# Performance work log

Hardware: AMD Instinct MI355X
Metric: run time of the kernel (lower is better)

## Reference

```python
import jax, jax.numpy as jnp
import numpy as np

N = 50000
P = 200000
L = 6
IN_DIM = 128
OUT_DIM = 128
HEADS = 4


def setup_inputs() -> dict:
    key = jax.random.key(0)
    ks = jax.random.split(key, 7)
    x = jax.random.normal(ks[0], (N, IN_DIM), dtype=jnp.float32)
    path_list = jax.random.randint(ks[1], (P, L), 0, N, dtype=jnp.int64)
    s = 0.1
    w_ih = jax.random.normal(ks[2], (3 * OUT_DIM, IN_DIM), dtype=jnp.float32) * s
    w_hh = jax.random.normal(ks[3], (3 * OUT_DIM, OUT_DIM), dtype=jnp.float32) * s
    b_ih = jax.random.normal(ks[4], (3 * OUT_DIM,), dtype=jnp.float32) * s
    b_hh = jax.random.normal(ks[5], (3 * OUT_DIM,), dtype=jnp.float32) * s
    a = jax.random.uniform(ks[6], (OUT_DIM, HEADS), dtype=jnp.float32) * 2.0 - 1.0
    return {"x": x, "path_list": path_list, "w_ih": w_ih, "w_hh": w_hh,
            "b_ih": b_ih, "b_hh": b_hh, "a": a}


def _gru_final_hidden(feats, w_ih, w_hh, b_ih, b_hh):
    # feats: [P, L, in_dim]; PyTorch GRU cell semantics, h0 = 0.
    out_dim = w_hh.shape[1]
    p = feats.shape[0]

    def step(h, xt):
        gi = xt @ w_ih.T + b_ih          # [P, 3*out]
        gh = h @ w_hh.T + b_hh           # [P, 3*out]
        ir, iz, i_n = jnp.split(gi, 3, axis=-1)
        hr, hz, h_n = jnp.split(gh, 3, axis=-1)
        r = jax.nn.sigmoid(ir + hr)
        z = jax.nn.sigmoid(iz + hz)
        n_cand = jnp.tanh(i_n + r * h_n)
        h_new = (1.0 - z) * n_cand + z * h
        return h_new, None

    h0 = jnp.zeros((p, out_dim), feats.dtype)
    xs = jnp.swapaxes(feats, 0, 1)       # [L, P, in_dim]
    h, _ = jax.lax.scan(step, h0, xs)
    return h                              # [P, out_dim]


def reference(x, path_list, w_ih, w_hh, b_ih, b_hh, a):
    n, out_dim = x.shape[0], w_hh.shape[1]
    heads = a.shape[1]
    # F.embedding(path_list, x): gather path features [P, L, in_dim]
    feats = x[path_list]
    path_emb = _gru_final_hidden(feats, w_ih, w_hh, b_ih, b_hh)       # [P, out]
    # unnormalized attention per head
    att_un = jnp.exp(jax.nn.leaky_relu(path_emb @ a, negative_slope=0.2))  # [P, H]
    row = path_list[:, -1]                                             # owner node of each path
    # M @ att_un : segment-sum over owner nodes
    att_sum = jax.ops.segment_sum(att_un, row, num_segments=n)         # [N, H]
    # M.t() @ (1/att_sum) : gather back to paths
    att_low = (1.0 / att_sum)[row]                                     # [P, H]
    att_n = att_un * att_low                                           # [P, H]
    # reshape(-1,1).repeat(1,out).reshape(P,-1): each head's scalar repeated out_dim times
    att_rep = jnp.repeat(att_n, out_dim, axis=1)                       # [P, H*out]
    emb_rep = jnp.tile(path_emb, (1, heads))                           # [P, H*out]
    path_att_emb = att_rep * emb_rep
    node_att_emb = jax.ops.segment_sum(path_att_emb, row, num_segments=n)  # [N, H*out]
    return node_att_emb
```

## Files before the change

### kernel.cpp

```cpp
#include <hip/hip_runtime.h>
#include <hip/hip_bf16.h>
#include <math.h>

#define NN 50000
#define PP 200000
#define LL 6
#define DD 128
#define HH 4

#define TM 32
#define NT 512
#define HPAD 132

typedef __attribute__((ext_vector_type(8))) short short8;
typedef __attribute__((ext_vector_type(4))) float f32x4;

struct f3 { float x, y, z; };

__device__ __forceinline__ unsigned short f2bf(float v) {
    __hip_bfloat16 h = __float2bfloat16(v);
    return *(unsigned short*)&h;
}
__device__ __forceinline__ float bf2f(unsigned short u) {
    union { unsigned int i; float f; } c; c.i = ((unsigned int)u) << 16; return c.f;
}
__device__ __forceinline__ float fast_rcp(float x) { return __builtin_amdgcn_rcpf(x); }
__device__ __forceinline__ float fast_sigmoid(float x) {
    return fast_rcp(1.f + __expf(-x));
}
__device__ __forceinline__ float fast_tanh(float x) {
    float e = __expf(-2.f * fabsf(x));
    float t = (1.f - e) * fast_rcp(1.f + e);
    return copysignf(t, x);
}

__global__ void prep_w_kernel(const float* __restrict__ w_hh,
                              unsigned short* __restrict__ whb) {
    int i = blockIdx.x * 256 + threadIdx.x;
    if (i < 3 * DD * DD) whb[i] = f2bf(w_hh[i]);
}

__global__ void histo_kernel(const int* __restrict__ path_list,
                             int* __restrict__ cnt) {
    int p = blockIdx.x * 256 + threadIdx.x;
    if (p < PP) atomicAdd(&cnt[path_list[p * LL + (LL - 1)]], 1);
}

__global__ void scan_kernel(const int* __restrict__ cnt,
                            int* __restrict__ offs,
                            int* __restrict__ cursor) {
    __shared__ int ls[256];
    const int t = threadIdx.x;
    const int chunk = (NN + 255) / 256;
    int s = 0;
    for (int j = 0; j < chunk; ++j) {
        int i = t + j * 256;
        if (i < NN) s += cnt[i];
    }
    ls[t] = s; __syncthreads();
    for (int off = 1; off < 256; off <<= 1) {
        int v = (t >= off) ? ls[t - off] : 0;
        __syncthreads();
        ls[t] += v;
        __syncthreads();
    }
    int run = (t == 0) ? 0 : ls[t - 1];
    for (int j = 0; j < chunk; ++j) {
        int i = t + j * 256;
        if (i < NN) { offs[i] = run; cursor[i] = run; run += cnt[i]; }
    }
}

__global__ void scatter_kernel(const int* __restrict__ path_list,
                               int* __restrict__ cursor,
                               int* __restrict__ sorted) {
    int p = blockIdx.x * 256 + threadIdx.x;
    if (p < PP) {
        int row = path_list[p * LL + (LL - 1)];
        int k = atomicAdd(&cursor[row], 1);
        sorted[k] = p;
    }
}

__global__ __launch_bounds__(512, 2)
void gi_gemm_kernel(const float* __restrict__ x,
                    const float* __restrict__ w_ih,
                    const float* __restrict__ b_ih,
                    const float* __restrict__ b_hh,
                    float* __restrict__ gi)
{
    const int tid  = threadIdx.x;
    const int lane = tid & 63;
    const int wave = tid >> 6;
    const int lcol = lane & 15;
    const int quad = lane >> 4;
    const int ko   = quad * 8;
    const int d    = wave * 16 + lcol;
    const int r0   = blockIdx.x * 64;

    short8 B[3][4];
    float bias[3];
    #pragma unroll
    for (int c = 0; c < 3; ++c) {
        int col = c * 128 + d;
        #pragma unroll
        for (int ks = 0; ks < 4; ++ks) {
            const float4* src = (const float4*)(w_ih + (size_t)col * 128 + ks * 32 + ko);
            float4 f0 = src[0], f1 = src[1];
            short8 b;
            b[0] = (short)f2bf(f0.x); b[1] = (short)f2bf(f0.y);
            b[2] = (short)f2bf(f0.z); b[3] = (short)f2bf(f0.w);
            b[4] = (short)f2bf(f1.x); b[5] = (short)f2bf(f1.y);
            b[6] = (short)f2bf(f1.z); b[7] = (short)f2bf(f1.w);
            B[c][ks] = b;
        }
        bias[c] = b_ih[col] + ((c < 2) ? b_hh[col] : 0.f);
    }

    f32x4 acc[3][4];
    #pragma unroll
    for (int c = 0; c < 3; ++c)
        #pragma unroll
        for (int rt = 0; rt < 4; ++rt)
            acc[c][rt] = (f32x4){bias[c], bias[c], bias[c], bias[c]};

    #pragma unroll
    for (int ks = 0; ks < 4; ++ks) {
        #pragma unroll
        for (int rt = 0; rt < 4; ++rt) {
            int row = r0 + rt * 16 + lcol;
            if (row >= NN) row = NN - 1;
            const float4* src = (const float4*)(x + (size_t)row * 128 + ks * 32 + ko);
            float4 f0 = src[0], f1 = src[1];
            short8 av;
            av[0] = (short)f2bf(f0.x); av[1] = (short)f2bf(f0.y);
            av[2] = (short)f2bf(f0.z); av[3] = (short)f2bf(f0.w);
            av[4] = (short)f2bf(f1.x); av[5] = (short)f2bf(f1.y);
            av[6] = (short)f2bf(f1.z); av[7] = (short)f2bf(f1.w);
            acc[0][rt] = __builtin_amdgcn_mfma_f32_16x16x32_bf16(av, B[0][ks], acc[0][rt], 0, 0, 0);
            acc[1][rt] = __builtin_amdgcn_mfma_f32_16x16x32_bf16(av, B[1][ks], acc[1][rt], 0, 0, 0);
            acc[2][rt] = __builtin_amdgcn_mfma_f32_16x16x32_bf16(av, B[2][ks], acc[2][rt], 0, 0, 0);
        }
    }

    #pragma unroll
    for (int rt = 0; rt < 4; ++rt)
        #pragma unroll
        for (int rr = 0; rr < 4; ++rr) {
            int row = r0 + rt * 16 + quad * 4 + rr;
            if (row < NN) {
                float* o = gi + (size_t)row * 384 + d * 3;
                o[0] = acc[0][rt][rr];
                o[1] = acc[1][rt][rr];
                o[2] = acc[2][rt][rr];
            }
        }
}

__global__ __launch_bounds__(NT, 4)
void gru_att_kernel(const float* __restrict__ gi,
                    const int*   __restrict__ path_list,
                    const unsigned short* __restrict__ whb,
                    const float* __restrict__ b_hh,
                    const float* __restrict__ a,
                    float* __restrict__ att_sum,
                    unsigned short* __restrict__ emb,
                    float* __restrict__ att_un_g)
{
    __shared__ __align__(16) unsigned char smem[25856];
    unsigned short* hs0    = (unsigned short*)smem;
    unsigned short* hs1    = (unsigned short*)(smem + 8192);
    float*          hs_f   = (float*)smem;
    float*          red_s  = (float*)(smem + 16896);
    int*            nodes_s= (int*)(smem + 25088);

    const int tid  = threadIdx.x;
    const int lane = tid & 63;
    const int wave = tid >> 6;
    const int lcol = lane & 15;
    const int quad = lane >> 4;
    const int d    = wave * 16 + lcol;
    const int p0   = blockIdx.x * TM;
    const int ko   = quad * 8;

    short8 Bh[3][4];
    #pragma unroll
    for (int c = 0; c < 3; ++c)
        #pragma unroll
        for (int ks = 0; ks < 4; ++ks)
            Bh[c][ks] = *(const short8*)(whb + (size_t)(c * DD + d) * DD + ks * 32 + ko);
    const float bhn = b_hh[d + 256];

    for (int i = tid; i < TM * LL; i += NT) nodes_s[i] = path_list[(size_t)p0 * LL + i];
    if (tid < TM * DD / 8)
        ((uint4*)hs0)[tid] = make_uint4(0u, 0u, 0u, 0u);

    float hreg[8];
    #pragma unroll
    for (int i = 0; i < 8; ++i) hreg[i] = 0.f;

    __syncthreads();

    #pragma unroll 1
    for (int t = 0; t < LL; ++t) {
        unsigned short* hr = (t & 1) ? hs1 : hs0;
        unsigned short* hw = (t & 1) ? hs0 : hs1;

        f3 g[8];
        #pragma unroll
        for (int rt = 0; rt < 2; ++rt)
            #pragma unroll
            for (int r = 0; r < 4; ++r) {
                const int p = rt * 16 + quad * 4 + r;
                const int node = nodes_s[p * LL + t];
                g[rt * 4 + r] = *(const f3*)(gi + (size_t)node * 384 + d * 3);
            }

        f32x4 accR[2], accZ[2], accH[2];
        #pragma unroll
        for (int rt = 0; rt < 2; ++rt) {
            accR[rt] = (f32x4){0.f, 0.f, 0.f, 0.f};
            accZ[rt] = (f32x4){0.f, 0.f, 0.f, 0.f};
            accH[rt] = (f32x4){bhn, bhn, bhn, bhn};
        }

        #pragma unroll
        for (int ks = 0; ks < 4; ++ks) {
            const int kb = ks * 4 + quad;
            #pragma unroll
            for (int rt = 0; rt < 2; ++rt) {
                const int p = rt * 16 + lcol;
                short8 ah = *(const short8*)(hr + p * DD + ((kb ^ lcol) * 8));
                accR[rt] = __builtin_amdgcn_mfma_f32_16x16x32_bf16(ah, Bh[0][ks], accR[rt], 0, 0, 0);
                accZ[rt] = __builtin_amdgcn_mfma_f32_16x16x32_bf16(ah, Bh[1][ks], accZ[rt], 0, 0, 0);
                accH[rt] = __builtin_amdgcn_mfma_f32_16x16x32_bf16(ah, Bh[2][ks], accH[rt], 0, 0, 0);
            }
        }

        if (t == LL - 1) __syncthreads();

        #pragma unroll
        for (int rt = 0; rt < 2; ++rt) {
            #pragma unroll
            for (int r = 0; r < 4; ++r) {
                const int idx = rt * 4 + r;
                const int p   = rt * 16 + quad * 4 + r;
                float rg = fast_sigmoid(accR[rt][r] + g[idx].x);
                float zg = fast_sigmoid(accZ[rt][r] + g[idx].y);
                float ng = fast_tanh(g[idx].z + rg * accH[rt][r]);
                float hnew = fmaf(zg, hreg[idx] - ng, ng);
                hreg[idx] = hnew;
                if (t < LL - 1) {
                    hw[p * DD + (((d >> 3) ^ (p & 15)) * 8) + (d & 7)] = f2bf(hnew);
                } else {
                    hs_f[p * HPAD + d] = hnew;
                }
            }
        }
        __syncthreads();
    }

    {
        int pi = tid >> 4, tt = tid & 15;
        float s0 = 0.f, s1 = 0.f, s2 = 0.f, s3 = 0.f;
        unsigned short pack[8];
        #pragma unroll
        for (int j = 0; j < 8; ++j) {
            int dd2 = tt * 8 + j;
            float hv = hs_f[pi * HPAD + dd2];
            pack[j] = f2bf(hv);
            float4 av = *(const float4*)(a + dd2 * 4);
            s0 += hv * av.x; s1 += hv * av.y; s2 += hv * av.z; s3 += hv * av.w;
        }
        *(uint4*)(emb + (size_t)(p0 + pi) * DD + tt * 8) = *(uint4*)&pack[0];
        float* rp = red_s + (pi * 16 + tt) * 4;
        rp[0] = s0; rp[1] = s1; rp[2] = s2; rp[3] = s3;
    }
    __syncthreads();
    if (tid < TM) {
        int pi = tid;
        int row = nodes_s[pi * LL + (LL - 1)];
        float4 e4;
        #pragma unroll
        for (int h = 0; h < HH; ++h) {
            float s = 0.f;
            #pragma unroll
            for (int tt = 0; tt < 16; ++tt) s += red_s[(pi * 16 + tt) * 4 + h];
            float lv = (s > 0.f) ? s : 0.2f * s;
            float e  = __expf(lv);
            ((float*)&e4)[h] = e;
            atomicAdd(&att_sum[row * HH + h], e);
        }
        *(float4*)(att_un_g + (size_t)(p0 + pi) * HH) = e4;
    }
}

__global__ __launch_bounds__(256)
void agg_kernel(const unsigned short* __restrict__ emb,
                const float* __restrict__ att_un,
                const float* __restrict__ att_sum,
                const int* __restrict__ offs,
                const int* __restrict__ cnt,
                const int* __restrict__ sorted,
                float* __restrict__ out)
{
    int node = blockIdx.x * 2 + (threadIdx.x >> 7);
    int d    = threadIdx.x & 127;
    if (node >= NN) return;
    int start = offs[node];
    int len   = cnt[node];
    float a0 = 0.f, a1 = 0.f, a2 = 0.f, a3 = 0.f;
    for (int i = 0; i < len; ++i) {
        int p = sorted[start + i];
        float4 at = *(const float4*)(att_un + (size_t)p * 4);
        float ev = bf2f(emb[(size_t)p * DD + d]);
        a0 = fmaf(at.x, ev, a0);
        a1 = fmaf(at.y, ev, a1);
        a2 = fmaf(at.z, ev, a2);
        a3 = fmaf(at.w, ev, a3);
    }
    float4 s = *(const float4*)(att_sum + (size_t)node * 4);
    float* o = out + (size_t)node * 512 + d;
    o[0]   = (s.x > 0.f) ? a0 / s.x : 0.f;
    o[128] = (s.y > 0.f) ? a1 / s.y : 0.f;
    o[256] = (s.z > 0.f) ? a2 / s.z : 0.f;
    o[384] = (s.w > 0.f) ? a3 / s.w : 0.f;
}

extern "C" void kernel_launch(void* const* d_in, const int* in_sizes, int n_in,
                              void* d_out, int out_size, void* d_ws, size_t ws_size,
                              hipStream_t stream) {
    const float* x         = (const float*)d_in[0];
    const int*   path_list = (const int*)  d_in[1];
    const float* w_ih      = (const float*)d_in[2];
    const float* w_hh      = (const float*)d_in[3];
    const float* b_ih      = (const float*)d_in[4];
    const float* b_hh      = (const float*)d_in[5];
    const float* a         = (const float*)d_in[6];
    float* out = (float*)d_out;

    char* w = (char*)d_ws;
    float*          att_sum = (float*)w;                 w += 800000;
    int*            cnt     = (int*)w;                   w += 200000;
    int*            offs    = (int*)w;                   w += 200000;
    int*            cursor  = (int*)w;                   w += 200000;
    int*            sorted  = (int*)w;                   w += 800000;
    float*          att_un  = (float*)w;                 w += 3200000;
    float*          gi      = (float*)w;                 w += 76800000;
    unsigned short* whb     = (unsigned short*)w;        w += 98304;
    unsigned short* emb     = (unsigned short*)w;        w += 51200000;

    hipMemsetAsync(att_sum, 0, 800000, stream);
    hipMemsetAsync(cnt, 0, 200000, stream);

    prep_w_kernel<<<(3 * DD * DD + 255) / 256, 256, 0, stream>>>(w_hh, whb);

    histo_kernel<<<(PP + 255) / 256, 256, 0, stream>>>(path_list, cnt);
    scan_kernel<<<1, 256, 0, stream>>>(cnt, offs, cursor);
    scatter_kernel<<<(PP + 255) / 256, 256, 0, stream>>>(path_list, cursor, sorted);

    gi_gemm_kernel<<<(NN + 63) / 64, 512, 0, stream>>>(x, w_ih, b_ih, b_hh, gi);

    gru_att_kernel<<<PP / TM, NT, 0, stream>>>(gi, path_list, whb,
                                               b_hh, a, att_sum, emb, att_un);

    agg_kernel<<<(NN + 1) / 2, 256, 0, stream>>>(emb, att_un, att_sum,
                                                 offs, cnt, sorted, out);
}
```

Measured before the change: 779.6 us.

## Split fused GRU recurrence into per-timestep kernels with global hidden state

Replaces the single kernel that ran all six GRU steps with LDS-resident hidden state by five launches, one per timestep. Each launch reloads the bf16 hidden state from global memory and writes it back. Step 0 is computed analytically in the first launch, since h0 is zero and no matmul is needed. The intent is likely to cut per-block LDS and loop overhead and to improve latency hiding across steps, at the cost of extra global traffic (about 51MB per step) and more launches.

```diff
diff --git a/kernel.cpp b/kernel.cpp
--- a/kernel.cpp
+++ b/kernel.cpp
@@ -157,22 +157,24 @@
         }
 }
 
-__global__ __launch_bounds__(NT, 4)
-void gru_att_kernel(const float* __restrict__ gi,
-                    const int*   __restrict__ path_list,
-                    const unsigned short* __restrict__ whb,
-                    const float* __restrict__ b_hh,
-                    const float* __restrict__ a,
-                    float* __restrict__ att_sum,
-                    unsigned short* __restrict__ emb,
-                    float* __restrict__ att_un_g)
+template <bool FIRST, bool LAST>
+__global__ __launch_bounds__(NT, 2)
+void gru_step_kernel(const float* __restrict__ gi,
+                     const int*   __restrict__ path_list,
+                     const unsigned short* __restrict__ whb,
+                     const float* __restrict__ b_hh,
+                     const float* __restrict__ a,
+                     unsigned short* __restrict__ H,
+                     float* __restrict__ att_sum,
+                     float* __restrict__ att_un_g,
+                     int t)
 {
-    __shared__ __align__(16) unsigned char smem[25856];
-    unsigned short* hs0    = (unsigned short*)smem;
-    unsigned short* hs1    = (unsigned short*)(smem + 8192);
-    float*          hs_f   = (float*)smem;
-    float*          red_s  = (float*)(smem + 16896);
-    int*            nodes_s= (int*)(smem + 25088);
+    constexpr int SM_BYTES = LAST ? 25216 : 8320;
+    __shared__ __align__(16) unsigned char smem[SM_BYTES];
+    unsigned short* hs      = (unsigned short*)smem;
+    float*          hs_f    = (float*)smem;
+    float*          red_s   = (float*)(smem + 16896);
+    int*            nodes_s = (int*)(smem + (LAST ? 25088 : 8192));
 
     const int tid  = threadIdx.x;
     const int lane = tid & 63;
@@ -191,107 +193,128 @@
             Bh[c][ks] = *(const short8*)(whb + (size_t)(c * DD + d) * DD + ks * 32 + ko);
     const float bhn = b_hh[d + 256];
 
-    for (int i = tid; i < TM * LL; i += NT) nodes_s[i] = path_list[(size_t)p0 * LL + i];
-    if (tid < TM * DD / 8)
-        ((uint4*)hs0)[tid] = make_uint4(0u, 0u, 0u, 0u);
-
-    float hreg[8];
-    #pragma unroll
-    for (int i = 0; i < 8; ++i) hreg[i] = 0.f;
-
+    {
+        const int gpi = tid >> 4;
+        const int tt  = tid & 15;
+        const int gpm = gpi & 15;
+        if (FIRST) {
+            int n0 = path_list[(size_t)(p0 + gpi) * LL + 0];
+            const float* gsrc = gi + (size_t)n0 * 384 + (tt * 8) * 3;
+            unsigned short pk[8];
+            #pragma unroll
+            for (int j = 0; j < 8; ++j) {
+                f3 gv = *(const f3*)(gsrc + j * 3);
+                int col = tt * 8 + j;
+                float rr = fast_sigmoid(gv.x);
+                float zz = fast_sigmoid(gv.y);
+                float nn = fast_tanh(gv.z + rr * b_hh[256 + col]);
+                pk[j] = f2bf((1.f - zz) * nn);
+            }
+            *(uint4*)(hs + gpi * DD + ((tt ^ gpm) * 8)) = *(uint4*)pk;
+        } else {
+            uint4 v = *(const uint4*)(H + (size_t)(p0 + gpi) * DD + tt * 8);
+            *(uint4*)(hs + gpi * DD + ((tt ^ gpm) * 8)) = v;
+        }
+    }
+    if (tid < TM) nodes_s[tid] = path_list[(size_t)(p0 + tid) * LL + t];
     __syncthreads();
 
-    #pragma unroll 1
-    for (int t = 0; t < LL; ++t) {
-        unsigned short* hr = (t & 1) ? hs1 : hs0;
-        unsigned short* hw = (t & 1) ? hs0 : hs1;
-
-        f3 g[8];
+    f3 g[8];
+    #pragma unroll
+    for (int rt = 0; rt < 2; ++rt)
+        #pragma unroll
+        for (int r = 0; r < 4; ++r) {
+            const int p = rt * 16 + quad * 4 + r;
+            g[rt * 4 + r] = *(const f3*)(gi + (size_t)nodes_s[p] * 384 + d * 3);
+        }
+
+    f32x4 accR[2], accZ[2], accH[2];
+    #pragma unroll
+    for (int rt = 0; rt < 2; ++rt) {
+        accR[rt] = (f32x4){0.f, 0.f, 0.f, 0.f};
+        accZ[rt] = (f32x4){0.f, 0.f, 0.f, 0.f};
+        accH[rt] = (f32x4){bhn, bhn, bhn, bhn};
+    }
+
+    #pragma unroll
+    for (int ks = 0; ks < 4; ++ks) {
+        const int kb = ks * 4 + quad;
+        #pragma unroll
+        for (int rt = 0; rt < 2; ++rt) {
+            const int p = rt * 16 + lcol;
+            short8 ah = *(const short8*)(hs + p * DD + ((kb ^ lcol) * 8));
+            accR[rt] = __builtin_amdgcn_mfma_f32_16x16x32_bf16(ah, Bh[0][ks], accR[rt], 0, 0, 0);
+            accZ[rt] = __builtin_amdgcn_mfma_f32_16x16x32_bf16(ah, Bh[1][ks], accZ[rt], 0, 0, 0);
+            accH[rt] = __builtin_amdgcn_mfma_f32_16x16x32_bf16(ah, Bh[2][ks], accH[rt], 0, 0, 0);
+        }
+    }
+
+    float hn8[8];
+    #pragma unroll
+    for (int rt = 0; rt < 2; ++rt)
+        #pragma unroll
+        for (int r = 0; r < 4; ++r) {
+            const int idx = rt * 4 + r;
+            const int p   = rt * 16 + quad * 4 + r;
+            float hprev = bf2f(hs[p * DD + (((d >> 3) ^ (p & 15)) * 8) + (d & 7)]);
+            float rg = fast_sigmoid(accR[rt][r] + g[idx].x);
+            float zg = fast_sigmoid(accZ[rt][r] + g[idx].y);
+            float ng = fast_tanh(g[idx].z + rg * accH[rt][r]);
+            hn8[idx] = fmaf(zg, hprev - ng, ng);
+        }
+
+    if (!LAST) {
         #pragma unroll
         for (int rt = 0; rt < 2; ++rt)
             #pragma unroll
             for (int r = 0; r < 4; ++r) {
                 const int p = rt * 16 + quad * 4 + r;
-                const int node = nodes_s[p * LL + t];
-                g[rt * 4 + r] = *(const f3*)(gi + (size_t)node * 384 + d * 3);
-            }
-
-        f32x4 accR[2], accZ[2], accH[2];
-        #pragma unroll
-        for (int rt = 0; rt < 2; ++rt) {
-            accR[rt] = (f32x4){0.f, 0.f, 0.f, 0.f};
-            accZ[rt] = (f32x4){0.f, 0.f, 0.f, 0.f};
-            accH[rt] = (f32x4){bhn, bhn, bhn, bhn};
-        }
-
-        #pragma unroll
-        for (int ks = 0; ks < 4; ++ks) {
-            const int kb = ks * 4 + quad;
-            #pragma unroll
-            for (int rt = 0; rt < 2; ++rt) {
-                const int p = rt * 16 + lcol;
-                short8 ah = *(const short8*)(hr + p * DD + ((kb ^ lcol) * 8));
-                accR[rt] = __builtin_amdgcn_mfma_f32_16x16x32_bf16(ah, Bh[0][ks], accR[rt], 0, 0, 0);
-                accZ[rt] = __builtin_amdgcn_mfma_f32_16x16x32_bf16(ah, Bh[1][ks], accZ[rt], 0, 0, 0);
-                accH[rt] = __builtin_amdgcn_mfma_f32_16x16x32_bf16(ah, Bh[2][ks], accH[rt], 0, 0, 0);
-            }
-        }
-
-        if (t == LL - 1) __syncthreads();
-
-        #pragma unroll
-        for (int rt = 0; rt < 2; ++rt) {
+                H[(size_t)(p0 + p) * DD + d] = f2bf(hn8[rt * 4 + r]);
+            }
+    } else {
+        __syncthreads();
+        #pragma unroll
+        for (int rt = 0; rt < 2; ++rt)
             #pragma unroll
             for (int r = 0; r < 4; ++r) {
-                const int idx = rt * 4 + r;
-                const int p   = rt * 16 + quad * 4 + r;
-                float rg = fast_sigmoid(accR[rt][r] + g[idx].x);
-                float zg = fast_sigmoid(accZ[rt][r] + g[idx].y);
-                float ng = fast_tanh(g[idx].z + rg * accH[rt][r]);
-                float hnew = fmaf(zg, hreg[idx] - ng, ng);
-                hreg[idx] = hnew;
-                if (t < LL - 1) {
-                    hw[p * DD + (((d >> 3) ^ (p & 15)) * 8) + (d & 7)] = f2bf(hnew);
-                } else {
-                    hs_f[p * HPAD + d] = hnew;
-                }
-            }
-        }
-        __syncthreads();
-    }
-
-    {
-        int pi = tid >> 4, tt = tid & 15;
-        float s0 = 0.f, s1 = 0.f, s2 = 0.f, s3 = 0.f;
-        unsigned short pack[8];
-        #pragma unroll
-        for (int j = 0; j < 8; ++j) {
-            int dd2 = tt * 8 + j;
-            float hv = hs_f[pi * HPAD + dd2];
-            pack[j] = f2bf(hv);
-            float4 av = *(const float4*)(a + dd2 * 4);
-            s0 += hv * av.x; s1 += hv * av.y; s2 += hv * av.z; s3 += hv * av.w;
-        }
-        *(uint4*)(emb + (size_t)(p0 + pi) * DD + tt * 8) = *(uint4*)&pack[0];
-        float* rp = red_s + (pi * 16 + tt) * 4;
-        rp[0] = s0; rp[1] = s1; rp[2] = s2; rp[3] = s3;
-    }
-    __syncthreads();
-    if (tid < TM) {
-        int pi = tid;
-        int row = nodes_s[pi * LL + (LL - 1)];
-        float4 e4;
-        #pragma unroll
-        for (int h = 0; h < HH; ++h) {
-            float s = 0.f;
-            #pragma unroll
-            for (int tt = 0; tt < 16; ++tt) s += red_s[(pi * 16 + tt) * 4 + h];
-            float lv = (s > 0.f) ? s : 0.2f * s;
-            float e  = __expf(lv);
-            ((float*)&e4)[h] = e;
-            atomicAdd(&att_sum[row * HH + h], e);
-        }
-        *(float4*)(att_un_g + (size_t)(p0 + pi) * HH) = e4;
+                const int p = rt * 16 + quad * 4 + r;
+                hs_f[p * HPAD + d] = hn8[rt * 4 + r];
+            }
+        __syncthreads();
+
+        {
+            int pi = tid >> 4, tt = tid & 15;
+            float s0 = 0.f, s1 = 0.f, s2 = 0.f, s3 = 0.f;
+            unsigned short pack[8];
+            #pragma unroll
+            for (int j = 0; j < 8; ++j) {
+                int dd2 = tt * 8 + j;
+                float hv = hs_f[pi * HPAD + dd2];
+                pack[j] = f2bf(hv);
+                float4 av = *(const float4*)(a + dd2 * 4);
+                s0 += hv * av.x; s1 += hv * av.y; s2 += hv * av.z; s3 += hv * av.w;
+            }
+            *(uint4*)(H + (size_t)(p0 + pi) * DD + tt * 8) = *(uint4*)&pack[0];
+            float* rp = red_s + (pi * 16 + tt) * 4;
+            rp[0] = s0; rp[1] = s1; rp[2] = s2; rp[3] = s3;
+        }
+        __syncthreads();
+        if (tid < TM) {
+            int pi = tid;
+            int row = nodes_s[pi];
+            float4 e4;
+            #pragma unroll
+            for (int h = 0; h < HH; ++h) {
+                float s = 0.f;
+                #pragma unroll
+                for (int tt = 0; tt < 16; ++tt) s += red_s[(pi * 16 + tt) * 4 + h];
+                float lv = (s > 0.f) ? s : 0.2f * s;
+                float e  = __expf(lv);
+                ((float*)&e4)[h] = e;
+                atomicAdd(&att_sum[row * HH + h], e);
+            }
+            *(float4*)(att_un_g + (size_t)(p0 + pi) * HH) = e4;
+        }
     }
 }
 
@@ -348,7 +371,7 @@
     float*          att_un  = (float*)w;                 w += 3200000;
     float*          gi      = (float*)w;                 w += 76800000;
     unsigned short* whb     = (unsigned short*)w;        w += 98304;
-    unsigned short* emb     = (unsigned short*)w;        w += 51200000;
+    unsigned short* H       = (unsigned short*)w;        w += 51200000;
 
     hipMemsetAsync(att_sum, 0, 800000, stream);
     hipMemsetAsync(cnt, 0, 200000, stream);
@@ -361,9 +384,12 @@
 
     gi_gemm_kernel<<<(NN + 63) / 64, 512, 0, stream>>>(x, w_ih, b_ih, b_hh, gi);
 
-    gru_att_kernel<<<PP / TM, NT, 0, stream>>>(gi, path_list, whb,
-                                               b_hh, a, att_sum, emb, att_un);
-
-    agg_kernel<<<(NN + 1) / 2, 256, 0, stream>>>(emb, att_un, att_sum,
+    gru_step_kernel<true,  false><<<PP / TM, NT, 0, stream>>>(gi, path_list, whb, b_hh, a, H, att_sum, att_un, 1);
+    gru_step_kernel<false, false><<<PP / TM, NT, 0, stream>>>(gi, path_list, whb, b_hh, a, H, att_sum, att_un, 2);
+    gru_step_kernel<false, false><<<PP / TM, NT, 0, stream>>>(gi, path_list, whb, b_hh, a, H, att_sum, att_un, 3);
+    gru_step_kernel<false, false><<<PP / TM, NT, 0, stream>>>(gi, path_list, whb, b_hh, a, H, att_sum, att_un, 4);
+    gru_step_kernel<false, true ><<<PP / TM, NT, 0, stream>>>(gi, path_list, whb, b_hh, a, H, att_sum, att_un, 5);
+
+    agg_kernel<<<(NN + 1) / 2, 256, 0, stream>>>(H, att_un, att_sum,
                                                  offs, cnt, sorted, out);
 }
```

After: 859.3 us. +10.2%, slower.
